# Kernel tuning notes

Measured on AMD Instinct MI355X. Metric: run time of the kernel, lower is better.

## Reference

```python
import jax, jax.numpy as jnp
import numpy as np

MODE_STATIC = 0
MODE_APPEARANCE_CHANGE = 2
MODE_BLINK = 3
MODE_AFFINE = 4


def _affine_warp(src, theta):
    """F.affine_grid + F.grid_sample(bilinear, zeros, align_corners=False).

    src:   [N, C, H, W]
    theta: [N, 2, 3]
    """
    N, C, H, W = src.shape
    dt = src.dtype
    # affine_grid base coords (align_corners=False): centers of pixels in [-1, 1]
    xs = (jnp.arange(W, dtype=dt) * 2 + 1) / W - 1  # [W]
    ys = (jnp.arange(H, dtype=dt) * 2 + 1) / H - 1  # [H]
    gx = (theta[:, 0, 0][:, None, None] * xs[None, None, :]
          + theta[:, 0, 1][:, None, None] * ys[None, :, None]
          + theta[:, 0, 2][:, None, None])  # [N, H, W]
    gy = (theta[:, 1, 0][:, None, None] * xs[None, None, :]
          + theta[:, 1, 1][:, None, None] * ys[None, :, None]
          + theta[:, 1, 2][:, None, None])  # [N, H, W]
    # unnormalize (align_corners=False)
    ix = ((gx + 1) * W - 1) / 2
    iy = ((gy + 1) * H - 1) / 2
    x0 = jnp.floor(ix)
    y0 = jnp.floor(iy)
    wx1 = ix - x0
    wy1 = iy - y0
    wx0 = 1 - wx1
    wy0 = 1 - wy1
    x0i = x0.astype(jnp.int32)
    y0i = y0.astype(jnp.int32)

    src_flat = src.reshape(N, C, H * W)

    def gather(xi, yi):
        valid = (xi >= 0) & (xi < W) & (yi >= 0) & (yi < H)  # zeros padding
        xi_c = jnp.clip(xi, 0, W - 1)
        yi_c = jnp.clip(yi, 0, H - 1)
        idx = (yi_c * W + xi_c).reshape(N, 1, H * W)
        v = jnp.take_along_axis(src_flat, idx, axis=2).reshape(N, C, H, W)
        return v * valid.astype(dt)[:, None]

    out = (gather(x0i, y0i) * (wx0 * wy0)[:, None]
           + gather(x0i + 1, y0i) * (wx1 * wy0)[:, None]
           + gather(x0i, y0i + 1) * (wx0 * wy1)[:, None]
           + gather(x0i + 1, y0i + 1) * (wx1 * wy1)[:, None])
    return out


def setup_inputs() -> dict:
    key = jax.random.key(0)
    ks = jax.random.split(key, 7)
    B, NI, C, H, W = 4, 16, 3, 256, 256
    g0 = jax.random.normal(ks[0], (B, NI, C, H, W), dtype=jnp.float32)
    m0 = jax.random.uniform(ks[1], (B, NI, 1, H, W), dtype=jnp.float32)
    mode_logits = jax.random.normal(ks[2], (B, NI, 5), dtype=jnp.float32)
    # near-identity affine transforms (realistic small motions)
    ident = jnp.array([1.0, 0.0, 0.0, 0.0, 1.0, 0.0], dtype=jnp.float32)
    transform_params = ident + 0.1 * jax.random.normal(ks[3], (B, NI, 6), dtype=jnp.float32)
    alpha = jax.random.uniform(ks[4], (B, NI, 1), dtype=jnp.float32)
    instance_valid = (jax.random.uniform(ks[5], (B, NI)) > 0.2).astype(jnp.float32)
    i_bg = jax.random.normal(ks[6], (B, C, H, W), dtype=jnp.float32)
    return {"g0": g0, "m0": m0, "mode_logits": mode_logits,
            "transform_params": transform_params, "alpha": alpha,
            "instance_valid": instance_valid, "i_bg": i_bg}


def reference(g0, m0, mode_logits, transform_params, alpha, instance_valid, i_bg):
    B, NI, C, H, W = g0.shape
    theta = transform_params.reshape(-1, 2, 3)  # [B*NI, 2, 3]
    warped_overlay = _affine_warp(g0.reshape(B * NI, C, H, W), theta).reshape(B, NI, C, H, W)
    warped_mask = _affine_warp(m0.reshape(B * NI, 1, H, W), theta).reshape(B, NI, 1, H, W)

    mode_ids = jnp.argmax(mode_logits, axis=-1)  # [B, NI]
    static_like = ((mode_ids == MODE_STATIC) | (mode_ids == MODE_APPEARANCE_CHANGE)
                   | (mode_ids == MODE_AFFINE)).astype(g0.dtype)[:, :, None, None, None]
    blink = (mode_ids == MODE_BLINK).astype(g0.dtype)[:, :, None, None, None]
    alpha_map = alpha[:, :, :, None, None]  # [B, NI, 1, 1, 1]
    valid = instance_valid[:, :, None, None, None]

    g_mid_per_instance = (static_like * warped_overlay + blink * warped_overlay * alpha_map) * valid
    m_mid_per_instance = (static_like * warped_mask + blink * warped_mask * alpha_map) * valid
    g_mid = g_mid_per_instance.sum(axis=1)
    m_mid = jnp.clip(m_mid_per_instance.sum(axis=1), 0.0, 1.0)
    i_base = i_bg + g_mid
    return (g_mid_per_instance, m_mid_per_instance, g_mid, m_mid, i_base)
```

## Files before the change

### kernel.cpp

```cpp
#include <hip/hip_runtime.h>

#define BB 4
#define NI 16
#define CC 3
#define HH 256
#define WW 256
#define HWSZ (HH * WW)

__global__ void prep_kernel(const float* __restrict__ ml,
                            const float* __restrict__ tp,
                            const float* __restrict__ al,
                            const float* __restrict__ iv,
                            float* __restrict__ wsf) {
    const int i = threadIdx.x;
    if (i >= BB * NI) return;
    float best = ml[i * 5];
    int bid = 0;
#pragma unroll
    for (int k = 1; k < 5; ++k) {
        float v = ml[i * 5 + k];
        if (v > best) { best = v; bid = k; }
    }
    float coef = (bid == 0 || bid == 2 || bid == 4) ? 1.0f
               : (bid == 3 ? al[i] : 0.0f);
    coef *= iv[i];
#pragma unroll
    for (int k = 0; k < 6; ++k) wsf[i * 8 + k] = tp[i * 6 + k];
    wsf[i * 8 + 6] = coef;
    wsf[i * 8 + 7] = 0.0f;
}

__global__ __launch_bounds__(256) void warp_inst(
    const float* __restrict__ g0,
    const float* __restrict__ m0,
    const float* __restrict__ wsf,
    float* __restrict__ out_gpi,
    float* __restrict__ out_mpi) {
    const int w = threadIdx.x;
    const int h = blockIdx.x;
    const int id = blockIdx.y;
    const int pix = h * WW + w;

    const float* p = wsf + id * 8;
    const float coef = p[6];

    float* gp = out_gpi + (size_t)id * CC * HWSZ + pix;
    float* mp = out_mpi + (size_t)id * HWSZ + pix;

    if (coef == 0.0f) {
        gp[0] = 0.0f; gp[HWSZ] = 0.0f; gp[2 * HWSZ] = 0.0f; mp[0] = 0.0f;
        return;
    }

    const float xs = (2 * w + 1) * (1.0f / WW) - 1.0f;
    const float ys = (2 * h + 1) * (1.0f / HH) - 1.0f;

    const float gx = p[0] * xs + p[1] * ys + p[2];
    const float gy = p[3] * xs + p[4] * ys + p[5];
    const float ix = gx * (0.5f * WW) + (0.5f * WW - 0.5f);
    const float iy = gy * (0.5f * HH) + (0.5f * HH - 0.5f);
    const float x0f = floorf(ix), y0f = floorf(iy);
    const float wx1 = ix - x0f, wy1 = iy - y0f;
    const float wx0 = 1.0f - wx1, wy0 = 1.0f - wy1;
    const int x0 = (int)x0f, y0 = (int)y0f;
    const bool vx0 = (unsigned)x0 < (unsigned)WW;
    const bool vx1 = (unsigned)(x0 + 1) < (unsigned)WW;
    const bool vy0 = (unsigned)y0 < (unsigned)HH;
    const bool vy1 = (unsigned)(y0 + 1) < (unsigned)HH;
    const bool v00 = vx0 && vy0, v10 = vx1 && vy0;
    const bool v01 = vx0 && vy1, v11 = vx1 && vy1;
    const int o00 = y0 * WW + x0;
    const float w00 = wx0 * wy0, w10 = wx1 * wy0;
    const float w01 = wx0 * wy1, w11 = wx1 * wy1;

    const float* gsrc = g0 + (size_t)id * CC * HWSZ;
    const float* msrc = m0 + (size_t)id * HWSZ;

    const float a00_0 = v00 ? gsrc[o00] : 0.0f;
    const float a10_0 = v10 ? gsrc[o00 + 1] : 0.0f;
    const float a01_0 = v01 ? gsrc[o00 + WW] : 0.0f;
    const float a11_0 = v11 ? gsrc[o00 + WW + 1] : 0.0f;
    const float a00_1 = v00 ? gsrc[HWSZ + o00] : 0.0f;
    const float a10_1 = v10 ? gsrc[HWSZ + o00 + 1] : 0.0f;
    const float a01_1 = v01 ? gsrc[HWSZ + o00 + WW] : 0.0f;
    const float a11_1 = v11 ? gsrc[HWSZ + o00 + WW + 1] : 0.0f;
    const float a00_2 = v00 ? gsrc[2 * HWSZ + o00] : 0.0f;
    const float a10_2 = v10 ? gsrc[2 * HWSZ + o00 + 1] : 0.0f;
    const float a01_2 = v01 ? gsrc[2 * HWSZ + o00 + WW] : 0.0f;
    const float a11_2 = v11 ? gsrc[2 * HWSZ + o00 + WW + 1] : 0.0f;
    const float m00 = v00 ? msrc[o00] : 0.0f;
    const float m10 = v10 ? msrc[o00 + 1] : 0.0f;
    const float m01 = v01 ? msrc[o00 + WW] : 0.0f;
    const float m11 = v11 ? msrc[o00 + WW + 1] : 0.0f;

    gp[0]        = coef * (w00 * a00_0 + w10 * a10_0 + w01 * a01_0 + w11 * a11_0);
    gp[HWSZ]     = coef * (w00 * a00_1 + w10 * a10_1 + w01 * a01_1 + w11 * a11_1);
    gp[2 * HWSZ] = coef * (w00 * a00_2 + w10 * a10_2 + w01 * a01_2 + w11 * a11_2);
    mp[0]        = coef * (w00 * m00 + w10 * m10 + w01 * m01 + w11 * m11);
}

__global__ __launch_bounds__(256) void combine_k(
    const float* __restrict__ gpi,
    const float* __restrict__ mpi,
    const float* __restrict__ i_bg,
    float* __restrict__ out_gmid,
    float* __restrict__ out_mmid,
    float* __restrict__ out_ibase) {
    const int w = threadIdx.x;
    const int h = blockIdx.x;
    const int b = blockIdx.y;
    const int pix = h * WW + w;

    float s0 = 0.f, s1 = 0.f, s2 = 0.f, sm = 0.f;
#pragma unroll
    for (int ii = 0; ii < NI; ++ii) {
        const size_t gb = (size_t)(b * NI + ii) * CC * HWSZ + pix;
        s0 += gpi[gb];
        s1 += gpi[gb + HWSZ];
        s2 += gpi[gb + 2 * HWSZ];
        sm += mpi[(size_t)(b * NI + ii) * HWSZ + pix];
    }
    const int ob = b * CC * HWSZ + pix;
    out_gmid[ob] = s0;
    out_gmid[ob + HWSZ] = s1;
    out_gmid[ob + 2 * HWSZ] = s2;
    out_ibase[ob] = s0 + i_bg[ob];
    out_ibase[ob + HWSZ] = s1 + i_bg[ob + HWSZ];
    out_ibase[ob + 2 * HWSZ] = s2 + i_bg[ob + 2 * HWSZ];
    out_mmid[b * HWSZ + pix] = fminf(fmaxf(sm, 0.0f), 1.0f);
}

extern "C" void kernel_launch(void* const* d_in, const int* in_sizes, int n_in,
                              void* d_out, int out_size, void* d_ws, size_t ws_size,
                              hipStream_t stream) {
    const float* g0          = (const float*)d_in[0];
    const float* m0          = (const float*)d_in[1];
    const float* mode_logits = (const float*)d_in[2];
    const float* tp          = (const float*)d_in[3];
    const float* alpha       = (const float*)d_in[4];
    const float* iv          = (const float*)d_in[5];
    const float* i_bg        = (const float*)d_in[6];

    float* out       = (float*)d_out;
    float* out_gpi   = out;
    float* out_mpi   = out_gpi  + (size_t)BB * NI * CC * HWSZ;
    float* out_gmid  = out_mpi  + (size_t)BB * NI * HWSZ;
    float* out_mmid  = out_gmid + (size_t)BB * CC * HWSZ;
    float* out_ibase = out_mmid + (size_t)BB * HWSZ;

    float* wsf = (float*)d_ws;

    prep_kernel<<<1, 64, 0, stream>>>(mode_logits, tp, alpha, iv, wsf);

    dim3 grid1(HH, BB * NI);
    warp_inst<<<grid1, WW, 0, stream>>>(g0, m0, wsf, out_gpi, out_mpi);

    dim3 grid2(HH, BB);
    combine_k<<<grid2, WW, 0, stream>>>(out_gpi, out_mpi, i_bg,
                                        out_gmid, out_mmid, out_ibase);
}
```

Before: 156.4 us.

## Inline param prep, vectorize warp stores and combine loads with float2/float4

Removes the separate prep kernel by computing argmax mode and coefficient inside each warp block. The warp kernel now handles two pixels per thread and writes float2 stores, and the combine kernel processes four pixels per thread with float4 loads and stores. This cuts one launch and reduces memory instruction count, at the cost of each thread recomputing the small per-instance parameters and lower thread counts per grid.

```diff
diff --git a/kernel.cpp b/kernel.cpp
--- a/kernel.cpp
+++ b/kernel.cpp
@@ -7,56 +7,37 @@
 #define WW 256
 #define HWSZ (HH * WW)
 
-__global__ void prep_kernel(const float* __restrict__ ml,
-                            const float* __restrict__ tp,
-                            const float* __restrict__ al,
-                            const float* __restrict__ iv,
-                            float* __restrict__ wsf) {
-    const int i = threadIdx.x;
-    if (i >= BB * NI) return;
-    float best = ml[i * 5];
+__device__ __forceinline__ float inst_params(
+    const float* __restrict__ ml, const float* __restrict__ tp,
+    const float* __restrict__ al, const float* __restrict__ iv,
+    int id, float th[6]) {
+    float best = ml[id * 5];
     int bid = 0;
 #pragma unroll
     for (int k = 1; k < 5; ++k) {
-        float v = ml[i * 5 + k];
+        float v = ml[id * 5 + k];
         if (v > best) { best = v; bid = k; }
     }
     float coef = (bid == 0 || bid == 2 || bid == 4) ? 1.0f
-               : (bid == 3 ? al[i] : 0.0f);
-    coef *= iv[i];
+               : (bid == 3 ? al[id] : 0.0f);
+    coef *= iv[id];
 #pragma unroll
-    for (int k = 0; k < 6; ++k) wsf[i * 8 + k] = tp[i * 6 + k];
-    wsf[i * 8 + 6] = coef;
-    wsf[i * 8 + 7] = 0.0f;
+    for (int k = 0; k < 6; ++k) th[k] = tp[id * 6 + k];
+    return coef;
 }
 
-__global__ __launch_bounds__(256) void warp_inst(
-    const float* __restrict__ g0,
-    const float* __restrict__ m0,
-    const float* __restrict__ wsf,
-    float* __restrict__ out_gpi,
-    float* __restrict__ out_mpi) {
-    const int w = threadIdx.x;
-    const int h = blockIdx.x;
-    const int id = blockIdx.y;
-    const int pix = h * WW + w;
+struct Samp {
+    int o00;
+    float w00, w10, w01, w11;
+    bool v00, v10, v01, v11;
+};
 
-    const float* p = wsf + id * 8;
-    const float coef = p[6];
-
-    float* gp = out_gpi + (size_t)id * CC * HWSZ + pix;
-    float* mp = out_mpi + (size_t)id * HWSZ + pix;
-
-    if (coef == 0.0f) {
-        gp[0] = 0.0f; gp[HWSZ] = 0.0f; gp[2 * HWSZ] = 0.0f; mp[0] = 0.0f;
-        return;
-    }
-
+__device__ __forceinline__ Samp make_samp(const float th[6], int p) {
+    const int h = p >> 8, w = p & (WW - 1);
     const float xs = (2 * w + 1) * (1.0f / WW) - 1.0f;
     const float ys = (2 * h + 1) * (1.0f / HH) - 1.0f;
-
-    const float gx = p[0] * xs + p[1] * ys + p[2];
-    const float gy = p[3] * xs + p[4] * ys + p[5];
+    const float gx = th[0] * xs + th[1] * ys + th[2];
+    const float gy = th[3] * xs + th[4] * ys + th[5];
     const float ix = gx * (0.5f * WW) + (0.5f * WW - 0.5f);
     const float iy = gy * (0.5f * HH) + (0.5f * HH - 0.5f);
     const float x0f = floorf(ix), y0f = floorf(iy);
@@ -67,67 +48,113 @@
     const bool vx1 = (unsigned)(x0 + 1) < (unsigned)WW;
     const bool vy0 = (unsigned)y0 < (unsigned)HH;
     const bool vy1 = (unsigned)(y0 + 1) < (unsigned)HH;
-    const bool v00 = vx0 && vy0, v10 = vx1 && vy0;
-    const bool v01 = vx0 && vy1, v11 = vx1 && vy1;
-    const int o00 = y0 * WW + x0;
-    const float w00 = wx0 * wy0, w10 = wx1 * wy0;
-    const float w01 = wx0 * wy1, w11 = wx1 * wy1;
+    Samp s;
+    s.o00 = y0 * WW + x0;
+    s.v00 = vx0 && vy0; s.v10 = vx1 && vy0;
+    s.v01 = vx0 && vy1; s.v11 = vx1 && vy1;
+    s.w00 = wx0 * wy0;  s.w10 = wx1 * wy0;
+    s.w01 = wx0 * wy1;  s.w11 = wx1 * wy1;
+    return s;
+}
+
+__device__ __forceinline__ float bilerp(const float* __restrict__ src, const Samp& s) {
+    const float a00 = s.v00 ? src[s.o00] : 0.0f;
+    const float a10 = s.v10 ? src[s.o00 + 1] : 0.0f;
+    const float a01 = s.v01 ? src[s.o00 + WW] : 0.0f;
+    const float a11 = s.v11 ? src[s.o00 + WW + 1] : 0.0f;
+    return s.w00 * a00 + s.w10 * a10 + s.w01 * a01 + s.w11 * a11;
+}
+
+__global__ __launch_bounds__(256) void warp_inst(
+    const float* __restrict__ g0,
+    const float* __restrict__ m0,
+    const float* __restrict__ ml,
+    const float* __restrict__ tp,
+    const float* __restrict__ al,
+    const float* __restrict__ iv,
+    float* __restrict__ out_gpi,
+    float* __restrict__ out_mpi) {
+    const int id = blockIdx.y;
+    const int p0 = blockIdx.x * 512 + threadIdx.x * 2;
+
+    float th[6];
+    const float coef = inst_params(ml, tp, al, iv, id, th);
+
+    float* gp = out_gpi + (size_t)id * CC * HWSZ + p0;
+    float* mp = out_mpi + (size_t)id * HWSZ + p0;
+
+    if (coef == 0.0f) {
+        const float2 z = make_float2(0.0f, 0.0f);
+        *(float2*)(gp)            = z;
+        *(float2*)(gp + HWSZ)     = z;
+        *(float2*)(gp + 2 * HWSZ) = z;
+        *(float2*)(mp)            = z;
+        return;
+    }
+
+    const Samp sa = make_samp(th, p0);
+    const Samp sb = make_samp(th, p0 + 1);
 
     const float* gsrc = g0 + (size_t)id * CC * HWSZ;
     const float* msrc = m0 + (size_t)id * HWSZ;
 
-    const float a00_0 = v00 ? gsrc[o00] : 0.0f;
-    const float a10_0 = v10 ? gsrc[o00 + 1] : 0.0f;
-    const float a01_0 = v01 ? gsrc[o00 + WW] : 0.0f;
-    const float a11_0 = v11 ? gsrc[o00 + WW + 1] : 0.0f;
-    const float a00_1 = v00 ? gsrc[HWSZ + o00] : 0.0f;
-    const float a10_1 = v10 ? gsrc[HWSZ + o00 + 1] : 0.0f;
-    const float a01_1 = v01 ? gsrc[HWSZ + o00 + WW] : 0.0f;
-    const float a11_1 = v11 ? gsrc[HWSZ + o00 + WW + 1] : 0.0f;
-    const float a00_2 = v00 ? gsrc[2 * HWSZ + o00] : 0.0f;
-    const float a10_2 = v10 ? gsrc[2 * HWSZ + o00 + 1] : 0.0f;
-    const float a01_2 = v01 ? gsrc[2 * HWSZ + o00 + WW] : 0.0f;
-    const float a11_2 = v11 ? gsrc[2 * HWSZ + o00 + WW + 1] : 0.0f;
-    const float m00 = v00 ? msrc[o00] : 0.0f;
-    const float m10 = v10 ? msrc[o00 + 1] : 0.0f;
-    const float m01 = v01 ? msrc[o00 + WW] : 0.0f;
-    const float m11 = v11 ? msrc[o00 + WW + 1] : 0.0f;
+    float2 r0, r1, r2, rm;
+    r0.x = coef * bilerp(gsrc, sa);
+    r0.y = coef * bilerp(gsrc, sb);
+    r1.x = coef * bilerp(gsrc + HWSZ, sa);
+    r1.y = coef * bilerp(gsrc + HWSZ, sb);
+    r2.x = coef * bilerp(gsrc + 2 * HWSZ, sa);
+    r2.y = coef * bilerp(gsrc + 2 * HWSZ, sb);
+    rm.x = coef * bilerp(msrc, sa);
+    rm.y = coef * bilerp(msrc, sb);
 
-    gp[0]        = coef * (w00 * a00_0 + w10 * a10_0 + w01 * a01_0 + w11 * a11_0);
-    gp[HWSZ]     = coef * (w00 * a00_1 + w10 * a10_1 + w01 * a01_1 + w11 * a11_1);
-    gp[2 * HWSZ] = coef * (w00 * a00_2 + w10 * a10_2 + w01 * a01_2 + w11 * a11_2);
-    mp[0]        = coef * (w00 * m00 + w10 * m10 + w01 * m01 + w11 * m11);
+    *(float2*)(gp)            = r0;
+    *(float2*)(gp + HWSZ)     = r1;
+    *(float2*)(gp + 2 * HWSZ) = r2;
+    *(float2*)(mp)            = rm;
 }
 
-__global__ __launch_bounds__(256) void combine_k(
+__global__ __launch_bounds__(128) void combine_k(
     const float* __restrict__ gpi,
     const float* __restrict__ mpi,
     const float* __restrict__ i_bg,
     float* __restrict__ out_gmid,
     float* __restrict__ out_mmid,
     float* __restrict__ out_ibase) {
-    const int w = threadIdx.x;
-    const int h = blockIdx.x;
     const int b = blockIdx.y;
-    const int pix = h * WW + w;
+    const int pix = (blockIdx.x * 128 + threadIdx.x) * 4;
 
-    float s0 = 0.f, s1 = 0.f, s2 = 0.f, sm = 0.f;
+    float4 s0 = make_float4(0.f, 0.f, 0.f, 0.f);
+    float4 s1 = s0, s2 = s0, sm = s0;
 #pragma unroll
     for (int ii = 0; ii < NI; ++ii) {
-        const size_t gb = (size_t)(b * NI + ii) * CC * HWSZ + pix;
-        s0 += gpi[gb];
-        s1 += gpi[gb + HWSZ];
-        s2 += gpi[gb + 2 * HWSZ];
-        sm += mpi[(size_t)(b * NI + ii) * HWSZ + pix];
+        const float* gb = gpi + (size_t)(b * NI + ii) * CC * HWSZ + pix;
+        const float4 a0 = *(const float4*)(gb);
+        const float4 a1 = *(const float4*)(gb + HWSZ);
+        const float4 a2 = *(const float4*)(gb + 2 * HWSZ);
+        const float4 am = *(const float4*)(mpi + (size_t)(b * NI + ii) * HWSZ + pix);
+        s0.x += a0.x; s0.y += a0.y; s0.z += a0.z; s0.w += a0.w;
+        s1.x += a1.x; s1.y += a1.y; s1.z += a1.z; s1.w += a1.w;
+        s2.x += a2.x; s2.y += a2.y; s2.z += a2.z; s2.w += a2.w;
+        sm.x += am.x; sm.y += am.y; sm.z += am.z; sm.w += am.w;
     }
-    const int ob = b * CC * HWSZ + pix;
-    out_gmid[ob] = s0;
-    out_gmid[ob + HWSZ] = s1;
-    out_gmid[ob + 2 * HWSZ] = s2;
-    out_ibase[ob] = s0 + i_bg[ob];
-    out_ibase[ob + HWSZ] = s1 + i_bg[ob + HWSZ];
-    out_ibase[ob + 2 * HWSZ] = s2 + i_bg[ob + 2 * HWSZ];
-    out_mmid[b * HWSZ + pix] = fminf(fmaxf(sm, 0.0f), 1.0f);
+    const size_t ob = (size_t)b * CC * HWSZ + pix;
+    const float4 bg0 = *(const float4*)(i_bg + ob);
+    const float4 bg1 = *(const float4*)(i_bg + ob + HWSZ);
+    const float4 bg2 = *(const float4*)(i_bg + ob + 2 * HWSZ);
+
+    *(float4*)(out_gmid + ob)            = s0;
+    *(float4*)(out_gmid + ob + HWSZ)     = s1;
+    *(float4*)(out_gmid + ob + 2 * HWSZ) = s2;
+    *(float4*)(out_ibase + ob) =
+        make_float4(s0.x + bg0.x, s0.y + bg0.y, s0.z + bg0.z, s0.w + bg0.w);
+    *(float4*)(out_ibase + ob + HWSZ) =
+        make_float4(s1.x + bg1.x, s1.y + bg1.y, s1.z + bg1.z, s1.w + bg1.w);
+    *(float4*)(out_ibase + ob + 2 * HWSZ) =
+        make_float4(s2.x + bg2.x, s2.y + bg2.y, s2.z + bg2.z, s2.w + bg2.w);
+    *(float4*)(out_mmid + (size_t)b * HWSZ + pix) =
+        make_float4(fminf(fmaxf(sm.x, 0.f), 1.f), fminf(fmaxf(sm.y, 0.f), 1.f),
+                    fminf(fmaxf(sm.z, 0.f), 1.f), fminf(fmaxf(sm.w, 0.f), 1.f));
 }
 
 extern "C" void kernel_launch(void* const* d_in, const int* in_sizes, int n_in,
@@ -148,14 +175,11 @@
     float* out_mmid  = out_gmid + (size_t)BB * CC * HWSZ;
     float* out_ibase = out_mmid + (size_t)BB * HWSZ;
 
-    float* wsf = (float*)d_ws;
+    dim3 grid1(HWSZ / 512, BB * NI);
+    warp_inst<<<grid1, 256, 0, stream>>>(g0, m0, mode_logits, tp, alpha, iv,
+                                         out_gpi, out_mpi);
 
-    prep_kernel<<<1, 64, 0, stream>>>(mode_logits, tp, alpha, iv, wsf);
-
-    dim3 grid1(HH, BB * NI);
-    warp_inst<<<grid1, WW, 0, stream>>>(g0, m0, wsf, out_gpi, out_mpi);
-
-    dim3 grid2(HH, BB);
-    combine_k<<<grid2, WW, 0, stream>>>(out_gpi, out_mpi, i_bg,
-                                        out_gmid, out_mmid, out_ibase);
+    dim3 grid2(HWSZ / 4 / 128, BB);
+    combine_k<<<grid2, 128, 0, stream>>>(out_gpi, out_mpi, i_bg,
+                                         out_gmid, out_mmid, out_ibase);
 }
```

After: 164.3 us. +5.1%, slower.
